# Kernel tuning notes

Measured on AMD Instinct MI355X. Metric: run time of the kernel, lower is better.

## Reference

```python
import jax, jax.numpy as jnp
import numpy as np

# dims
B, L, IN, H, OUT = 2, 2048, 128, 512, 64
NL, ED, N, DR, K = 2, 1024, 16, 32, 4  # n_layers, d_inner=2*H, d_state, dt_rank=ceil(H/16), d_conv


def setup_inputs() -> dict:
    key = jax.random.key(0)
    ks = jax.random.split(key, 18)
    r = lambda k, s: 0.05 * jax.random.normal(k, s, dtype=jnp.float32)
    return {
        "x": jax.random.normal(ks[0], (B, L, IN), dtype=jnp.float32),
        # LiquidNet proj (in_dim -> hidden -> hidden)
        "p_Wi": r(ks[1], (IN, H)), "p_bi": r(ks[2], (H,)), "p_bh": r(ks[3], (H,)),
        "p_Wo": r(ks[4], (H, H)), "p_bo": r(ks[5], (H,)),
        # Mamba layers (stacked over layer axis)
        "m_norm_w": jnp.ones((NL, H), jnp.float32),
        "m_in_W": r(ks[6], (NL, H, 2 * ED)),
        "m_conv_w": r(ks[7], (NL, ED, K)), "m_conv_b": r(ks[8], (NL, ED)),
        "m_xproj_W": r(ks[9], (NL, ED, DR + 2 * N)),
        "m_dt_W": r(ks[10], (NL, DR, ED)), "m_dt_b": r(ks[11], (NL, ED)),
        "m_A_log": jnp.tile(jnp.log(jnp.arange(1, N + 1, dtype=jnp.float32)), (NL, ED, 1)),
        "m_D": jnp.ones((NL, ED), jnp.float32),
        "m_out_W": r(ks[12], (NL, ED, H)),
        # LiquidNet dense (hidden -> out_dim -> out_dim)
        "d_Wi": r(ks[13], (H, OUT)), "d_bi": r(ks[14], (OUT,)), "d_bh": r(ks[15], (OUT,)),
        "d_Wo": r(ks[16], (OUT, OUT)), "d_bo": r(ks[17], (OUT,)),
    }


def _rmsnorm(x, w, eps=1e-5):
    return x * jax.lax.rsqrt(jnp.mean(x * x, axis=-1, keepdims=True) + eps) * w


def _liquid(x, Wi, bi, bh, Wo, bo):
    # liquid cell with zero initial hidden state: h = tanh(i2h(x) + h2h(0))
    h = jnp.tanh(x @ Wi + bi + bh)
    return h @ Wo + bo


def _causal_conv(x, w, b):
    # x: [B, L, ED]; depthwise causal conv with kernel K
    xt = x.transpose(0, 2, 1)  # [B, ED, L]
    y = jax.lax.conv_general_dilated(xt, w[:, None, :], (1,), [(K - 1, 0)],
                                     dimension_numbers=('NCH', 'OIH', 'NCH'),
                                     feature_group_count=ED)
    return (y + b[None, :, None]).transpose(0, 2, 1)


def _ssm(xc, delta, Bm, Cm, A, D):
    # xc/delta: [B,L,ED]; Bm/Cm: [B,L,N]; A: [ED,N]; D: [ED]
    deltaA = jnp.exp(delta[..., None] * A)                              # [B,L,ED,N]
    deltaBx = delta[..., None] * Bm[:, :, None, :] * xc[..., None]      # [B,L,ED,N]

    def step(h, t):
        dA, dBx, Ct = t
        h = dA * h + dBx
        return h, jnp.einsum('bdn,bn->bd', h, Ct)

    h0 = jnp.zeros((xc.shape[0], ED, N), xc.dtype)
    _, ys = jax.lax.scan(step, h0, (deltaA.transpose(1, 0, 2, 3),
                                    deltaBx.transpose(1, 0, 2, 3),
                                    Cm.transpose(1, 0, 2)))
    return ys.transpose(1, 0, 2) + D * xc


def _mamba_block(x, norm_w, in_W, conv_w, conv_b, xproj_W, dt_W, dt_b, A_log, D, out_W):
    xn = _rmsnorm(x, norm_w)
    xz = xn @ in_W                       # [B,L,2*ED]
    xc, z = jnp.split(xz, 2, axis=-1)
    xc = jax.nn.silu(_causal_conv(xc, conv_w, conv_b))
    dbl = xc @ xproj_W                   # [B,L,DR+2N]
    dt, Bm, Cm = dbl[..., :DR], dbl[..., DR:DR + N], dbl[..., DR + N:]
    delta = jax.nn.softplus(dt @ dt_W + dt_b)
    y = _ssm(xc, delta, Bm, Cm, -jnp.exp(A_log), D)
    y = y * jax.nn.silu(z)
    return y @ out_W


def reference(x, p_Wi, p_bi, p_bh, p_Wo, p_bo,
              m_norm_w, m_in_W, m_conv_w, m_conv_b, m_xproj_W, m_dt_W, m_dt_b,
              m_A_log, m_D, m_out_W,
              d_Wi, d_bi, d_bh, d_Wo, d_bo):
    out = _liquid(x, p_Wi, p_bi, p_bh, p_Wo, p_bo)
    for l in range(NL):  # residual Mamba blocks
        out = out + _mamba_block(out, m_norm_w[l], m_in_W[l], m_conv_w[l], m_conv_b[l],
                                 m_xproj_W[l], m_dt_W[l], m_dt_b[l], m_A_log[l], m_D[l], m_out_W[l])
    out = _liquid(out, d_Wi, d_bi, d_bh, d_Wo, d_bo)
    out = out - jnp.tanh(out)  # Tanhshrink
    return out.reshape(-1)
```

## Files before the change

kernel.cpp:

```cpp
#include <hip/hip_runtime.h>
#include <hip/hip_bf16.h>
#include <cstdint>
#include <cstddef>

#define B_   2
#define L_   2048
#define IN_  128
#define H_   512
#define OUT_ 64
#define NL_  2
#define ED_  1024
#define N_   16
#define DR_  32
#define K_   4

static constexpr int M_TOK = B_ * L_;
static constexpr int SEG   = 64;
static constexpr int TS    = L_ / SEG;

typedef __attribute__((ext_vector_type(8))) short bhalf8;
typedef __attribute__((ext_vector_type(4))) float floatx4;

__device__ __forceinline__ ushort bf16bits(float f)
{
    __hip_bfloat16 h = __float2bfloat16(f);
    return *reinterpret_cast<ushort*>(&h);
}

__device__ __forceinline__ void gld_lds16(const ushort* g, ushort* l)
{
    __builtin_amdgcn_global_load_lds(
        (const __attribute__((address_space(1))) unsigned int*)g,
        (__attribute__((address_space(3))) unsigned int*)l, 16, 0, 0);
}

template<int BM, int BN, int BK, int EPI, bool DUAL>
__global__ __launch_bounds__(256)
void mfma_gemm(const ushort* __restrict__ A, int lda,
               const ushort* Bt, int ldb,
               const ushort* Bt2, float* C2,
               const float* __restrict__ b1, const float* __restrict__ b2,
               float* C, __hip_bfloat16* Cb, int ldc,
               int M, int N, int kc)
{
    __shared__ __align__(16) ushort As[BM * BK];
    __shared__ __align__(16) ushort Bs[BN * BK];

    const int tid  = threadIdx.x;
    const int bm   = blockIdx.x * BM, bn = blockIdx.y * BN;
    int kz = 0, kbeg = 0;
    if (DUAL) {
        if (blockIdx.z) { Bt = Bt2; C = C2; }
    } else {
        kz = blockIdx.z; kbeg = kz * kc;
    }
    const int lane = tid & 63, wave = tid >> 6;
    const int wr = wave >> 1, wc = wave & 1;
    constexpr int WM = BM / 2, WN = BN / 2;
    constexpr int FM = WM / 16, FN = WN / 16;
    const int fr = lane & 15, fg = lane >> 4;

    constexpr int ACH = BM * BK / 512;
    constexpr int BCH = BN * BK / 512;
    constexpr int RPC = 512 / BK;
    constexpr int LPR = BK / 8;
    const int sr = lane / LPR;
    const int sc = (lane % LPR) * 8;

    floatx4 acc[FM][FN] = {};

    for (int k0 = kbeg; k0 < kbeg + kc; k0 += BK) {
        #pragma unroll
        for (int i = 0; i < ACH / 4; ++i) {
            const int ci = wave * (ACH / 4) + i;
            const int r  = ci * RPC + sr;
            gld_lds16(&A[(size_t)(bm + r) * lda + k0 + sc], &As[ci * 512]);
        }
        #pragma unroll
        for (int i = 0; i < BCH / 4; ++i) {
            const int ci = wave * (BCH / 4) + i;
            const int r  = ci * RPC + sr;
            gld_lds16(&Bt[(size_t)(bn + r) * ldb + k0 + sc], &Bs[ci * 512]);
        }
        __syncthreads();
        #pragma unroll
        for (int kk = 0; kk < BK; kk += 32) {
            bhalf8 fa[FM], fb[FN];
            #pragma unroll
            for (int m = 0; m < FM; ++m)
                fa[m] = *reinterpret_cast<const bhalf8*>(
                    &As[(wr * WM + m * 16 + fr) * BK + kk + fg * 8]);
            #pragma unroll
            for (int n = 0; n < FN; ++n)
                fb[n] = *reinterpret_cast<const bhalf8*>(
                    &Bs[(wc * WN + n * 16 + fr) * BK + kk + fg * 8]);
            #pragma unroll
            for (int m = 0; m < FM; ++m)
                #pragma unroll
                for (int n = 0; n < FN; ++n)
                    acc[m][n] = __builtin_amdgcn_mfma_f32_16x16x32_bf16(
                        fa[m], fb[n], acc[m][n], 0, 0, 0);
        }
        __syncthreads();
    }

    #pragma unroll
    for (int m = 0; m < FM; ++m) {
        #pragma unroll
        for (int n = 0; n < FN; ++n) {
            const int row0 = bm + wr * WM + m * 16 + fg * 4;
            const int col  = bn + wc * WN + n * 16 + fr;
            #pragma unroll
            for (int r = 0; r < 4; ++r) {
                float v = acc[m][n][r];
                const int row = row0 + r;
                if (EPI == 0) {
                    C[(size_t)row * ldc + col] = v;
                } else if (EPI == 1) {
                    C[(size_t)row * ldc + col] += v;
                } else if (EPI == 2) {
                    Cb[(size_t)row * ldc + col] =
                        __float2bfloat16(tanhf(v + b1[col] + b2[col]));
                } else if (EPI == 3) {
                    C[(size_t)row * ldc + col] = v + b1[col];
                } else if (EPI == 4) {
                    C[(size_t)kz * M * N + (size_t)row * N + col] = v;
                } else if (EPI == 5) {
                    const float w = v + b1[col];
                    C[(size_t)row * ldc + col] = w - tanhf(w);
                } else if (EPI == 6) {
                    const float w = v + b1[col];
                    C[(size_t)row * ldc + col] =
                        fmaxf(w, 0.0f) + log1pf(expf(-fabsf(w)));
                } else if (EPI == 7) {
                    float* cp = C + (size_t)row * ldc + col;
                    const float w = *cp + v;
                    *cp = w;
                    Cb[(size_t)row * ldc + col] = __float2bfloat16(w);
                }
            }
        }
    }
}

__global__ __launch_bounds__(256)
void xproj_gemm(const float* __restrict__ xcr,
                const float* __restrict__ cw, const float* __restrict__ cb,
                const ushort* __restrict__ Bt,
                float* __restrict__ Cpart)
{
    __shared__ __align__(16) ushort As[128 * 64];
    __shared__ __align__(16) ushort Bs[64 * 64];

    const int tid = threadIdx.x;
    const int bm  = blockIdx.x * 128;
    const int kz  = blockIdx.z;
    const int lane = tid & 63, wave = tid >> 6;
    const int wr = wave >> 1, wc = wave & 1;
    const int fr = lane & 15, fg = lane >> 4;
    const int tseq0 = bm & (L_ - 1);

    const int col8 = (tid & 7) * 8;
    const int rq   = tid >> 3;
    const int sr   = lane / 8, sc2 = (lane & 7) * 8;

    floatx4 acc[4][2] = {};

    #pragma unroll
    for (int ks = 0; ks < 2; ++ks) {
        const int k0 = kz * 128 + ks * 64;

        float4 wv[8]; float cbv[8];
        #pragma unroll
        for (int j = 0; j < 8; ++j) {
            wv[j]  = *reinterpret_cast<const float4*>(&cw[(k0 + col8 + j) * 4]);
            cbv[j] = cb[k0 + col8 + j];
        }
        float xr[7][8];
        #pragma unroll
        for (int ii = 0; ii < 7; ++ii) {
            const int tok = bm + rq * 4 - 3 + ii;
            const int tokc = tok < 0 ? 0 : tok;
            const float4 a = *reinterpret_cast<const float4*>(
                &xcr[(size_t)tokc * ED_ + k0 + col8]);
            const float4 b = *reinterpret_cast<const float4*>(
                &xcr[(size_t)tokc * ED_ + k0 + col8 + 4]);
            xr[ii][0]=a.x; xr[ii][1]=a.y; xr[ii][2]=a.z; xr[ii][3]=a.w;
            xr[ii][4]=b.x; xr[ii][5]=b.y; xr[ii][6]=b.z; xr[ii][7]=b.w;
        }
        #pragma unroll
        for (int rr = 0; rr < 4; ++rr) {
            const int trow = tseq0 + rq * 4 + rr;
            __align__(16) ushort ob[8];
            #pragma unroll
            for (int j = 0; j < 8; ++j) {
                float a = cbv[j] + wv[j].w * xr[rr + 3][j];
                if (trow >= 1) a += wv[j].z * xr[rr + 2][j];
                if (trow >= 2) a += wv[j].y * xr[rr + 1][j];
                if (trow >= 3) a += wv[j].x * xr[rr + 0][j];
                const float s = a / (1.0f + __expf(-a));
                ob[j] = bf16bits(s);
            }
            *reinterpret_cast<uint4*>(&As[(rq * 4 + rr) * 64 + col8]) =
                *reinterpret_cast<const uint4*>(ob);
        }
        #pragma unroll
        for (int i = 0; i < 2; ++i) {
            const int ci = wave * 2 + i;
            const int r  = ci * 8 + sr;
            gld_lds16(&Bt[(size_t)r * ED_ + k0 + sc2], &Bs[ci * 512]);
        }
        __syncthreads();
        #pragma unroll
        for (int kk = 0; kk < 64; kk += 32) {
            bhalf8 fa[4], fb[2];
            #pragma unroll
            for (int m = 0; m < 4; ++m)
                fa[m] = *reinterpret_cast<const bhalf8*>(
                    &As[(wr * 64 + m * 16 + fr) * 64 + kk + fg * 8]);
            #pragma unroll
            for (int n = 0; n < 2; ++n)
                fb[n] = *reinterpret_cast<const bhalf8*>(
                    &Bs[(wc * 32 + n * 16 + fr) * 64 + kk + fg * 8]);
            #pragma unroll
            for (int m = 0; m < 4; ++m)
                #pragma unroll
                for (int n = 0; n < 2; ++n)
                    acc[m][n] = __builtin_amdgcn_mfma_f32_16x16x32_bf16(
                        fa[m], fb[n], acc[m][n], 0, 0, 0);
        }
        __syncthreads();
    }

    #pragma unroll
    for (int m = 0; m < 4; ++m) {
        #pragma unroll
        for (int n = 0; n < 2; ++n) {
            const int row0 = bm + wr * 64 + m * 16 + fg * 4;
            const int col  = wc * 32 + n * 16 + fr;
            #pragma unroll
            for (int r = 0; r < 4; ++r)
                Cpart[(size_t)kz * M_TOK * 64 + (size_t)(row0 + r) * 64 + col] =
                    acc[m][n][r];
        }
    }
}

template<int NP, int ACT, bool B1, bool B2, int OUTMODE>
__global__ __launch_bounds__(256)
void reduce_part_k(const float* __restrict__ P, const float* __restrict__ b1,
                   const float* __restrict__ b2, float* __restrict__ Of,
                   __hip_bfloat16* __restrict__ Ob, int MN, int Ncols)
{
    const int i = blockIdx.x * 256 + threadIdx.x;
    float s = 0.0f;
    #pragma unroll
    for (int z = 0; z < NP; ++z) s += P[(size_t)z * MN + i];
    const int col = i & (Ncols - 1);
    if (B1) s += b1[col];
    if (B2) s += b2[col];
    if (ACT == 1) s = tanhf(s);
    if (OUTMODE == 0 || OUTMODE == 2) Of[i] = s;
    if (OUTMODE == 1 || OUTMODE == 2) Ob[i] = __float2bfloat16(s);
}

__device__ __forceinline__ void tr32(float (*t)[33],
                                     const float* __restrict__ W,
                                     __hip_bfloat16* __restrict__ Wt,
                                     int K, int N, int local, int gx, int tid)
{
    const int kx = local % gx, ny = local / gx;
    const int k0 = kx * 32, n0 = ny * 32;
    const int c = tid & 31, r4 = tid >> 5;
    #pragma unroll
    for (int i = 0; i < 4; ++i) {
        const int rr = r4 + i * 8;
        t[rr][c] = W[(size_t)(k0 + rr) * N + n0 + c];
    }
    __syncthreads();
    #pragma unroll
    for (int i = 0; i < 4; ++i) {
        const int rr = r4 + i * 8;
        Wt[(size_t)(n0 + rr) * K + k0 + c] = __float2bfloat16(t[c][rr]);
    }
}

__global__ __launch_bounds__(256)
void prep_k(const float* __restrict__ x, __hip_bfloat16* __restrict__ Xb,
            const float* pWi, __hip_bfloat16* TpWi,
            const float* pWo, __hip_bfloat16* TpWo,
            const float* inW, __hip_bfloat16* TinW0, __hip_bfloat16* TinW1,
            const float* xpW, __hip_bfloat16* TxpW0, __hip_bfloat16* TxpW1,
            const float* outW, __hip_bfloat16* ToutW0, __hip_bfloat16* ToutW1,
            const float* dWi, __hip_bfloat16* TdWi,
            const float* dtW, __hip_bfloat16* TdtW0, __hip_bfloat16* TdtW1,
            const float* dWo, __hip_bfloat16* TdWo)
{
    __shared__ float t[32][33];
    const int tid = threadIdx.x;
    int r = blockIdx.x;

    if (r < 512) {
        const int i = (r * 256 + tid) * 4;
        const float4 v = *reinterpret_cast<const float4*>(&x[i]);
        ushort4 u;
        u.x = bf16bits(v.x); u.y = bf16bits(v.y);
        u.z = bf16bits(v.z); u.w = bf16bits(v.w);
        *reinterpret_cast<ushort4*>(&Xb[i]) = u;
        return;
    }
    r -= 512;
    if (r < 64)   { tr32(t, pWi, TpWi, IN_, H_, r, 4, tid); return; }   r -= 64;
    if (r < 256)  { tr32(t, pWo, TpWo, H_, H_, r, 16, tid); return; }   r -= 256;
    if (r < 1024) { tr32(t, inW, TinW0, H_, 2 * ED_, r, 16, tid); return; } r -= 1024;
    if (r < 1024) { tr32(t, inW + (size_t)H_ * 2 * ED_, TinW1, H_, 2 * ED_, r, 16, tid); return; } r -= 1024;
    if (r < 64)   { tr32(t, xpW, TxpW0, ED_, 64, r, 32, tid); return; } r -= 64;
    if (r < 64)   { tr32(t, xpW + (size_t)ED_ * 64, TxpW1, ED_, 64, r, 32, tid); return; } r -= 64;
    if (r < 512)  { tr32(t, outW, ToutW0, ED_, H_, r, 32, tid); return; } r -= 512;
    if (r < 512)  { tr32(t, outW + (size_t)ED_ * H_, ToutW1, ED_, H_, r, 32, tid); return; } r -= 512;
    if (r < 32)   { tr32(t, dWi, TdWi, H_, OUT_, r, 16, tid); return; } r -= 32;
    if (r < 32)   { tr32(t, dtW, TdtW0, DR_, ED_, r, 1, tid); return; } r -= 32;
    if (r < 32)   { tr32(t, dtW + DR_ * ED_, TdtW1, DR_, ED_, r, 1, tid); return; } r -= 32;
    tr32(t, dWo, TdWo, OUT_, OUT_, r, 2, tid);
}
static constexpr int PREP_BLOCKS = 512 + 64 + 256 + 1024 + 1024 + 64 + 64 + 512 + 512 + 32 + 32 + 32 + 4;

__global__ __launch_bounds__(256)
void rmsnorm_k(const float* __restrict__ x, const float* __restrict__ w,
               __hip_bfloat16* __restrict__ o)
{
    const int row = blockIdx.x;
    const int tid = threadIdx.x;
    const float* xr = x + (size_t)row * H_;
    float v0 = xr[tid], v1 = xr[tid + 256];
    float s = v0 * v0 + v1 * v1;
    #pragma unroll
    for (int off = 32; off > 0; off >>= 1) s += __shfl_down(s, off, 64);
    __shared__ float ps[4];
    __shared__ float scale_s;
    const int wave = tid >> 6, lane = tid & 63;
    if (lane == 0) ps[wave] = s;
    __syncthreads();
    if (tid == 0) {
        float tot = ps[0] + ps[1] + ps[2] + ps[3];
        scale_s = rsqrtf(tot * (1.0f / H_) + 1e-5f);
    }
    __syncthreads();
    const float sc = scale_s;
    o[(size_t)row * H_ + tid]       = __float2bfloat16(v0 * sc * w[tid]);
    o[(size_t)row * H_ + tid + 256] = __float2bfloat16(v1 * sc * w[tid + 256]);
}

template<bool P3>
__global__ __launch_bounds__(256)
void ssm_scan_k(const float* __restrict__ delta,
                const float* __restrict__ xcr,
                const float* __restrict__ dbl,
                const float* __restrict__ cw, const float* __restrict__ cb,
                const float* __restrict__ zbuf,
                const float* __restrict__ A_log,
                const float* __restrict__ Dv,
                float* __restrict__ hend, float* __restrict__ pprod,
                const float* __restrict__ hinit,
                __hip_bfloat16* __restrict__ ybuf)
{
    __shared__ float sdl[TS][64];
    __shared__ float sxc[TS][64];
    __shared__ float bc[TS][32];

    const int bx   = blockIdx.x;
    const int seg  = bx & (SEG - 1);
    const int dblk = (bx >> 6) & 15;
    const int b    = bx >> 10;
    const int tid  = threadIdx.x;
    const int dbase = dblk * 64;
    const int t0   = seg * TS;
    const size_t row0 = (size_t)(b * L_ + t0);
    const int dls = tid & 63;

    #pragma unroll
    for (int e = 0; e < 8; ++e) {
        const int t = (tid >> 6) + e * 4;
        sdl[t][dls] = delta[(row0 + t) * ED_ + dbase + dls];
    }
    {
        const int tg = tid >> 6;
        const int tb = tg * 8;
        float xr[11];
        #pragma unroll
        for (int ii = 0; ii < 11; ++ii) {
            const int gt = t0 + tb - 3 + ii;
            xr[ii] = (gt >= 0)
                ? xcr[((size_t)(b * L_) + gt) * ED_ + dbase + dls] : 0.0f;
        }
        const float4 w = *reinterpret_cast<const float4*>(&cw[(dbase + dls) * 4]);
        const float cbv = cb[dbase + dls];
        #pragma unroll
        for (int k = 0; k < 8; ++k) {
            const float a = cbv + w.x * xr[k] + w.y * xr[k + 1]
                          + w.z * xr[k + 2] + w.w * xr[k + 3];
            sxc[tb + k][dls] = a / (1.0f + __expf(-a));
        }
    }
    #pragma unroll
    for (int e = 0; e < 4; ++e) {
        const int lin = tid + e * 256;
        bc[lin >> 5][lin & 31] = dbl[(row0 + (lin >> 5)) * 64 + 32 + (lin & 31)];
    }
    __syncthreads();

    const int dl = tid >> 2;
    const int ng = tid & 3;
    const int d  = dbase + dl;

    float Av[4];
    #pragma unroll
    for (int i = 0; i < 4; ++i) Av[i] = -expf(A_log[d * N_ + ng * 4 + i]);

    float h[4];
    float S = 0.0f;
    if (P3) {
        #pragma unroll
        for (int i = 0; i < 4; ++i)
            h[i] = hinit[((size_t)(b * SEG + seg) * N_ + ng * 4 + i) * ED_ + d];
    } else {
        #pragma unroll
        for (int i = 0; i < 4; ++i) h[i] = 0.0f;
    }
    const float Dd = P3 ? Dv[d] : 0.0f;

    #pragma unroll
    for (int t = 0; t < TS; ++t) {
        const float dvt = sdl[t][dl];
        const float xvt = sxc[t][dl];
        const float dx  = dvt * xvt;
        if (!P3) S += dvt;
        float ysum = 0.0f;
        #pragma unroll
        for (int i = 0; i < 4; ++i) {
            const float dA = __expf(dvt * Av[i]);
            h[i] = fmaf(dA, h[i], dx * bc[t][ng * 4 + i]);
            if (P3) ysum = fmaf(h[i], bc[t][16 + ng * 4 + i], ysum);
        }
        if (P3) {
            float y2 = ysum + __shfl_xor(ysum, 1, 64);
            float y4 = y2 + __shfl_xor(y2, 2, 64);
            if (ng == 0) {
                const float zv = zbuf[(row0 + t) * ED_ + d];
                const float sz = zv / (1.0f + __expf(-zv));
                ybuf[(row0 + t) * ED_ + d] =
                    __float2bfloat16((y4 + Dd * xvt) * sz);
            }
        }
    }

    if (!P3) {
        #pragma unroll
        for (int i = 0; i < 4; ++i) {
            const size_t o = ((size_t)(b * SEG + seg) * N_ + ng * 4 + i) * ED_ + d;
            hend[o]  = h[i];
            pprod[o] = __expf(Av[i] * S);
        }
    }
}

__global__ __launch_bounds__(256)
void ssm_combine_k(const float* __restrict__ hend, const float* __restrict__ pprod,
                   float* __restrict__ hinit)
{
    const int gid = blockIdx.x * 256 + threadIdx.x;
    const int d = gid & (ED_ - 1);
    const int n = (gid >> 10) & (N_ - 1);
    const int b = gid >> 14;
    size_t o = ((size_t)(b * SEG) * N_ + n) * ED_ + d;
    const size_t stride = (size_t)N_ * ED_;
    float h = 0.0f;
    #pragma unroll 8
    for (int s = 0; s < SEG; ++s) {
        hinit[o] = h;
        h = fmaf(pprod[o], h, hend[o]);
        o += stride;
    }
}

extern "C" void kernel_launch(void* const* d_in, const int* in_sizes, int n_in,
                              void* d_out, int out_size, void* d_ws, size_t ws_size,
                              hipStream_t stream)
{
    const float* x      = (const float*)d_in[0];
    const float* p_Wi   = (const float*)d_in[1];
    const float* p_bi   = (const float*)d_in[2];
    const float* p_bh   = (const float*)d_in[3];
    const float* p_Wo   = (const float*)d_in[4];
    const float* p_bo   = (const float*)d_in[5];
    const float* m_norm = (const float*)d_in[6];
    const float* m_inW  = (const float*)d_in[7];
    const float* m_cw   = (const float*)d_in[8];
    const float* m_cb   = (const float*)d_in[9];
    const float* m_xpW  = (const float*)d_in[10];
    const float* m_dtW  = (const float*)d_in[11];
    const float* m_dtb  = (const float*)d_in[12];
    const float* m_Alog = (const float*)d_in[13];
    const float* m_D    = (const float*)d_in[14];
    const float* m_outW = (const float*)d_in[15];
    const float* d_Wi   = (const float*)d_in[16];
    const float* d_bi   = (const float*)d_in[17];
    const float* d_bh   = (const float*)d_in[18];
    const float* d_Wo   = (const float*)d_in[19];
    const float* d_bo   = (const float*)d_in[20];
    float* out_f = (float*)d_out;
    float* ws = (float*)d_ws;

    float* OUT   = ws;
    float* XCR   = ws + 2097152;
    float* Z     = ws + 6291456;
    float* DELTA = ws + 10485760;
    float* HEND  = ws + 14680064;
    float* PPROD = ws + 16777216;
    float* HINIT = ws + 18874368;
    float* BF    = ws + 20971520;
    float* WT    = ws + 23068672;
    float* DBL   = ws + 24922112;
    float* DBLF  = ws + 25184256;

    float* CPARTX = HEND;
    float* CPART2 = XCR;
    __hip_bfloat16* Xb   = (__hip_bfloat16*)BF;
    __hip_bfloat16* H1b  = (__hip_bfloat16*)(BF + 262144);
    __hip_bfloat16* XNb  = (__hip_bfloat16*)BF;
    __hip_bfloat16* YB   = (__hip_bfloat16*)BF;
    __hip_bfloat16* H2b  = (__hip_bfloat16*)DBL;
    __hip_bfloat16* OUTb = (__hip_bfloat16*)PPROD;
    __hip_bfloat16* DBLb = (__hip_bfloat16*)DBLF;

    __hip_bfloat16* WTu     = (__hip_bfloat16*)WT;
    __hip_bfloat16* T_pWi   = WTu;
    __hip_bfloat16* T_pWo   = WTu + 65536;
    __hip_bfloat16* T_inW0  = WTu + 327680;
    __hip_bfloat16* T_inW1  = WTu + 1376256;
    __hip_bfloat16* T_xpW0  = WTu + 2424832;
    __hip_bfloat16* T_xpW1  = WTu + 2490368;
    __hip_bfloat16* T_outW0 = WTu + 2555904;
    __hip_bfloat16* T_outW1 = WTu + 3080192;
    __hip_bfloat16* T_dWi   = WTu + 3604480;
    __hip_bfloat16* T_dtW0  = WTu + 3637248;
    __hip_bfloat16* T_dtW1  = WTu + 3670016;
    __hip_bfloat16* T_dWo   = WTu + 3702784;

    const dim3 blk(256);

    prep_k<<<dim3(PREP_BLOCKS), blk, 0, stream>>>(
        x, Xb, p_Wi, T_pWi, p_Wo, T_pWo, m_inW, T_inW0, T_inW1,
        m_xpW, T_xpW0, T_xpW1, m_outW, T_outW0, T_outW1,
        d_Wi, T_dWi, m_dtW, T_dtW0, T_dtW1, d_Wo, T_dWo);

    mfma_gemm<128, 64, 64, 2, false><<<dim3(32, 8), blk, 0, stream>>>(
        (const ushort*)Xb, IN_, (const ushort*)T_pWi, IN_, nullptr, nullptr,
        p_bi, p_bh, nullptr, H1b, H_, M_TOK, H_, IN_);
    mfma_gemm<128, 64, 64, 3, false><<<dim3(32, 8), blk, 0, stream>>>(
        (const ushort*)H1b, H_, (const ushort*)T_pWo, H_, nullptr, nullptr,
        p_bo, nullptr, OUT, nullptr, H_, M_TOK, H_, H_);

    for (int l = 0; l < NL_; ++l) {
        const float* nw   = m_norm + l * H_;
        const float* cw   = m_cw   + l * ED_ * K_;
        const float* cb   = m_cb   + l * ED_;
        const float* dtb  = m_dtb  + l * ED_;
        const float* Alog = m_Alog + l * ED_ * N_;
        const float* Dv   = m_D    + l * ED_;
        const __hip_bfloat16* TinW  = l ? T_inW1  : T_inW0;
        const __hip_bfloat16* TxpW  = l ? T_xpW1  : T_xpW0;
        const __hip_bfloat16* ToutW = l ? T_outW1 : T_outW0;
        const __hip_bfloat16* TdtW  = l ? T_dtW1  : T_dtW0;

        rmsnorm_k<<<dim3(M_TOK), blk, 0, stream>>>(OUT, nw, XNb);
        mfma_gemm<128, 128, 64, 0, true><<<dim3(32, 8, 2), blk, 0, stream>>>(
            (const ushort*)XNb, H_, (const ushort*)TinW, H_,
            (const ushort*)(TinW + (size_t)ED_ * H_), Z,
            nullptr, nullptr, XCR, nullptr, ED_, M_TOK, ED_, H_);
        xproj_gemm<<<dim3(32, 1, 8), blk, 0, stream>>>(
            XCR, cw, cb, (const ushort*)TxpW, CPARTX);
        reduce_part_k<8, 0, false, false, 2><<<dim3(1024), blk, 0, stream>>>(
            CPARTX, nullptr, nullptr, DBL, DBLb, M_TOK * 64, 64);
        mfma_gemm<128, 64, 32, 6, false><<<dim3(32, 16), blk, 0, stream>>>(
            (const ushort*)DBLb, 64, (const ushort*)TdtW, DR_, nullptr, nullptr,
            dtb, nullptr, DELTA, nullptr, ED_, M_TOK, ED_, DR_);
        ssm_scan_k<false><<<dim3(2048), blk, 0, stream>>>(
            DELTA, XCR, DBL, cw, cb, nullptr, Alog, nullptr,
            HEND, PPROD, nullptr, nullptr);
        ssm_combine_k<<<dim3(128), blk, 0, stream>>>(HEND, PPROD, HINIT);
        ssm_scan_k<true><<<dim3(2048), blk, 0, stream>>>(
            DELTA, XCR, DBL, cw, cb, Z, Alog, Dv,
            nullptr, nullptr, HINIT, YB);
        if (l == 0) {
            mfma_gemm<128, 64, 64, 1, false><<<dim3(32, 8), blk, 0, stream>>>(
                (const ushort*)YB, ED_, (const ushort*)ToutW, ED_, nullptr, nullptr,
                nullptr, nullptr, OUT, nullptr, H_, M_TOK, H_, ED_);
        } else {
            mfma_gemm<128, 64, 64, 7, false><<<dim3(32, 8), blk, 0, stream>>>(
                (const ushort*)YB, ED_, (const ushort*)ToutW, ED_, nullptr, nullptr,
                nullptr, nullptr, OUT, OUTb, H_, M_TOK, H_, ED_);
        }
    }

    mfma_gemm<128, 64, 64, 4, false><<<dim3(32, 1, 8), blk, 0, stream>>>(
        (const ushort*)OUTb, H_, (const ushort*)T_dWi, H_, nullptr, nullptr,
        nullptr, nullptr, CPART2, nullptr, 64, M_TOK, 64, H_ / 8);
    reduce_part_k<8, 1, true, true, 1><<<dim3(1024), blk, 0, stream>>>(
        CPART2, d_bi, d_bh, nullptr, H2b, M_TOK * 64, 64);
    mfma_gemm<128, 64, 64, 5, false><<<dim3(32, 1), blk, 0, stream>>>(
        (const ushort*)H2b, OUT_, (const ushort*)T_dWo, OUT_, nullptr, nullptr,
        d_bo, nullptr, out_f, nullptr, OUT_, M_TOK, OUT_, OUT_);
}
```

Measured before the change: 327.7 us.

## Fuse SSM chunked scan passes into one cooperative kernel with grid syncs

Replaces the three-kernel SSM sequence (per-segment scan, cross-segment combine, second scan with output) with one cooperative kernel. Between phases it uses grid-wide syncs and keeps the delta, conv/silu x and B/C tiles in shared memory, so the second pass neither reloads them nor recomputes the conv. Two kernel launches and the global re-reads are removed. In exchange it needs all 2048 blocks co-resident (8 per CU), adds grid barrier cost, and has only 128 blocks do the serial combine while the rest wait.

```diff
diff --git a/kernel.cpp b/kernel.cpp
--- a/kernel.cpp
+++ b/kernel.cpp
@@ -1,7 +1,10 @@
 #include <hip/hip_runtime.h>
 #include <hip/hip_bf16.h>
+#include <hip/hip_cooperative_groups.h>
 #include <cstdint>
 #include <cstddef>
+
+namespace cg = cooperative_groups;
 
 #define B_   2
 #define L_   2048
@@ -351,6 +354,143 @@
     o[(size_t)row * H_ + tid + 256] = __float2bfloat16(v1 * sc * w[tid + 256]);
 }
 
+__global__ __launch_bounds__(256, 8)
+void ssm_mega_k(const float* __restrict__ delta,
+                const float* __restrict__ xcr,
+                const float* __restrict__ dbl,
+                const float* __restrict__ cw, const float* __restrict__ cb,
+                const float* __restrict__ zbuf,
+                const float* __restrict__ A_log,
+                const float* __restrict__ Dv,
+                float* __restrict__ hend, float* __restrict__ pprod,
+                float* __restrict__ hinit,
+                __hip_bfloat16* __restrict__ ybuf)
+{
+    __shared__ float sdl[TS][64];
+    __shared__ float sxc[TS][64];
+    __shared__ float bc[TS][32];
+
+    const int bx   = blockIdx.x;
+    const int seg  = bx & (SEG - 1);
+    const int dblk = (bx >> 6) & 15;
+    const int b    = bx >> 10;
+    const int tid  = threadIdx.x;
+    const int dbase = dblk * 64;
+    const int t0   = seg * TS;
+    const size_t row0 = (size_t)(b * L_ + t0);
+    const int dls = tid & 63;
+
+    #pragma unroll
+    for (int e = 0; e < 8; ++e) {
+        const int t = (tid >> 6) + e * 4;
+        sdl[t][dls] = delta[(row0 + t) * ED_ + dbase + dls];
+    }
+    {
+        const int tg = tid >> 6;
+        const int tb = tg * 8;
+        float xr[11];
+        #pragma unroll
+        for (int ii = 0; ii < 11; ++ii) {
+            const int gt = t0 + tb - 3 + ii;
+            xr[ii] = (gt >= 0)
+                ? xcr[((size_t)(b * L_) + gt) * ED_ + dbase + dls] : 0.0f;
+        }
+        const float4 w = *reinterpret_cast<const float4*>(&cw[(dbase + dls) * 4]);
+        const float cbv = cb[dbase + dls];
+        #pragma unroll
+        for (int k = 0; k < 8; ++k) {
+            const float a = cbv + w.x * xr[k] + w.y * xr[k + 1]
+                          + w.z * xr[k + 2] + w.w * xr[k + 3];
+            sxc[tb + k][dls] = a / (1.0f + __expf(-a));
+        }
+    }
+    #pragma unroll
+    for (int e = 0; e < 4; ++e) {
+        const int lin = tid + e * 256;
+        bc[lin >> 5][lin & 31] = dbl[(row0 + (lin >> 5)) * 64 + 32 + (lin & 31)];
+    }
+    __syncthreads();
+
+    const int dl = tid >> 2;
+    const int ng = tid & 3;
+    const int d  = dbase + dl;
+
+    float Av[4];
+    #pragma unroll
+    for (int i = 0; i < 4; ++i) Av[i] = -expf(A_log[d * N_ + ng * 4 + i]);
+    const float Dd = Dv[d];
+
+    {
+        float h[4] = {0.0f, 0.0f, 0.0f, 0.0f};
+        float S = 0.0f;
+        #pragma unroll
+        for (int t = 0; t < TS; ++t) {
+            const float dvt = sdl[t][dl];
+            const float dx  = dvt * sxc[t][dl];
+            S += dvt;
+            #pragma unroll
+            for (int i = 0; i < 4; ++i) {
+                const float dA = __expf(dvt * Av[i]);
+                h[i] = fmaf(dA, h[i], dx * bc[t][ng * 4 + i]);
+            }
+        }
+        #pragma unroll
+        for (int i = 0; i < 4; ++i) {
+            const size_t o = ((size_t)(b * SEG + seg) * N_ + ng * 4 + i) * ED_ + d;
+            hend[o]  = h[i];
+            pprod[o] = __expf(Av[i] * S);
+        }
+    }
+
+    cg::this_grid().sync();
+
+    if (bx < 128) {
+        const int gid = bx * 256 + tid;
+        const int dd = gid & (ED_ - 1);
+        const int nn = (gid >> 10) & (N_ - 1);
+        const int bb = gid >> 14;
+        size_t o = ((size_t)(bb * SEG) * N_ + nn) * ED_ + dd;
+        const size_t stride = (size_t)N_ * ED_;
+        float hh = 0.0f;
+        #pragma unroll 8
+        for (int s = 0; s < SEG; ++s) {
+            hinit[o] = hh;
+            hh = fmaf(pprod[o], hh, hend[o]);
+            o += stride;
+        }
+    }
+
+    cg::this_grid().sync();
+
+    {
+        float h[4];
+        #pragma unroll
+        for (int i = 0; i < 4; ++i)
+            h[i] = hinit[((size_t)(b * SEG + seg) * N_ + ng * 4 + i) * ED_ + d];
+        #pragma unroll
+        for (int t = 0; t < TS; ++t) {
+            const float dvt = sdl[t][dl];
+            const float xvt = sxc[t][dl];
+            const float dx  = dvt * xvt;
+            float ysum = 0.0f;
+            #pragma unroll
+            for (int i = 0; i < 4; ++i) {
+                const float dA = __expf(dvt * Av[i]);
+                h[i] = fmaf(dA, h[i], dx * bc[t][ng * 4 + i]);
+                ysum = fmaf(h[i], bc[t][16 + ng * 4 + i], ysum);
+            }
+            float y2 = ysum + __shfl_xor(ysum, 1, 64);
+            float y4 = y2 + __shfl_xor(y2, 2, 64);
+            if (ng == 0) {
+                const float zv = zbuf[(row0 + t) * ED_ + d];
+                const float sz = zv / (1.0f + __expf(-zv));
+                ybuf[(row0 + t) * ED_ + d] =
+                    __float2bfloat16((y4 + Dd * xvt) * sz);
+            }
+        }
+    }
+}
+
 template<bool P3>
 __global__ __launch_bounds__(256)
 void ssm_scan_k(const float* __restrict__ delta,
@@ -549,6 +689,19 @@
 
     const dim3 blk(256);
 
+    int coop_ok = 0;
+    {
+        int dev = 0, attr = 0;
+        if (hipGetDevice(&dev) == hipSuccess &&
+            hipDeviceGetAttribute(&attr, hipDeviceAttributeCooperativeLaunch,
+                                  dev) == hipSuccess && attr) {
+            int nb = 0;
+            if (hipOccupancyMaxActiveBlocksPerMultiprocessor(
+                    &nb, ssm_mega_k, 256, 0) == hipSuccess && nb >= 8)
+                coop_ok = 1;
+        }
+    }
+
     prep_k<<<dim3(PREP_BLOCKS), blk, 0, stream>>>(
         x, Xb, p_Wi, T_pWi, p_Wo, T_pWo, m_inW, T_inW0, T_inW1,
         m_xpW, T_xpW0, T_xpW1, m_outW, T_outW0, T_outW1,
@@ -585,13 +738,28 @@
         mfma_gemm<128, 64, 32, 6, false><<<dim3(32, 16), blk, 0, stream>>>(
             (const ushort*)DBLb, 64, (const ushort*)TdtW, DR_, nullptr, nullptr,
             dtb, nullptr, DELTA, nullptr, ED_, M_TOK, ED_, DR_);
-        ssm_scan_k<false><<<dim3(2048), blk, 0, stream>>>(
-            DELTA, XCR, DBL, cw, cb, nullptr, Alog, nullptr,
-            HEND, PPROD, nullptr, nullptr);
-        ssm_combine_k<<<dim3(128), blk, 0, stream>>>(HEND, PPROD, HINIT);
-        ssm_scan_k<true><<<dim3(2048), blk, 0, stream>>>(
-            DELTA, XCR, DBL, cw, cb, Z, Alog, Dv,
-            nullptr, nullptr, HINIT, YB);
+
+        if (coop_ok) {
+            const float* a0 = DELTA;  const float* a1 = XCR;
+            const float* a2 = DBL;    const float* a3 = cw;
+            const float* a4 = cb;     const float* a5 = Z;
+            const float* a6 = Alog;   const float* a7 = Dv;
+            float* a8 = HEND;  float* a9 = PPROD;  float* a10 = HINIT;
+            __hip_bfloat16* a11 = YB;
+            void* args[12] = {&a0, &a1, &a2, &a3, &a4, &a5,
+                              &a6, &a7, &a8, &a9, &a10, &a11};
+            hipLaunchCooperativeKernel((void*)ssm_mega_k, dim3(2048), blk,
+                                       args, 0, stream);
+        } else {
+            ssm_scan_k<false><<<dim3(2048), blk, 0, stream>>>(
+                DELTA, XCR, DBL, cw, cb, nullptr, Alog, nullptr,
+                HEND, PPROD, nullptr, nullptr);
+            ssm_combine_k<<<dim3(128), blk, 0, stream>>>(HEND, PPROD, HINIT);
+            ssm_scan_k<true><<<dim3(2048), blk, 0, stream>>>(
+                DELTA, XCR, DBL, cw, cb, Z, Alog, Dv,
+                nullptr, nullptr, HINIT, YB);
+        }
+
         if (l == 0) {
             mfma_gemm<128, 64, 64, 1, false><<<dim3(32, 8), blk, 0, stream>>>(
                 (const ushort*)YB, ED_, (const ushort*)ToutW, ED_, nullptr, nullptr,
```

After: 328.2 us. No clear change (+0.2%).
